# Performance work log

Measured on AMD Instinct MI355X. Metric: run time of the kernel, lower is better.

The kernel has to match this reference:

```python
import jax, jax.numpy as jnp
import numpy as np

BS, NE, NN, CIN, H, D = 8, 4800, 4981, 3, 128, 6
EPG = 19200
NEDGE = BS * EPG
N = BS * NE

PARAM_NAMES = [
    'enc_cw1','enc_cb1','enc_cw2','enc_cb2','enc_cw3','enc_clng','enc_clnb',
    'enc_ew1','enc_eb1','enc_ew2','enc_eb2','enc_ew3','enc_elng','enc_elnb',
    'p_ew1','p_eb1','p_ew2','p_eb2','p_ew3','p_elng','p_elnb',
    'p_nw1','p_nb1','p_nw2','p_nb2','p_nw3','p_nlng','p_nlnb',
    'dec_uw1','dec_ub1','dec_uw2','dec_ub2','dec_uw3','dec_ulng','dec_ulnb',
    'dec_cw1','dec_cb1','dec_cw2','dec_cb2','dec_cw3']


def setup_inputs():
    key = jax.random.key(0)
    ks = iter(jax.random.split(key, 64))
    def nrm(shape, s=0.1):
        return jax.random.normal(next(ks), shape, jnp.float32) * s
    inp = {}
    inp['x'] = jax.random.normal(next(ks), (BS * NN, CIN), jnp.float32)
    inp['elem_conn'] = jax.random.randint(next(ks), (NE, 4), 0, NN)
    inp['edge_index'] = jax.random.randint(next(ks), (2, NEDGE), 0, N)
    inp['enc_cw1'] = nrm((CIN, 4, 1)); inp['enc_cb1'] = nrm((CIN, 1), 0.01)
    inp['enc_cw2'] = nrm((CIN, 1, 1)); inp['enc_cb2'] = nrm((CIN, 1), 0.01)
    inp['enc_cw3'] = nrm((CIN, 1, 1))
    inp['enc_clng'] = jnp.ones((CIN, 1)); inp['enc_clnb'] = jnp.zeros((CIN, 1))
    inp['enc_ew1'] = nrm((CIN, H)); inp['enc_eb1'] = nrm((H,), 0.01)
    inp['enc_ew2'] = nrm((H, H)); inp['enc_eb2'] = nrm((H,), 0.01)
    inp['enc_ew3'] = nrm((H, H))
    inp['enc_elng'] = jnp.ones((H,)); inp['enc_elnb'] = jnp.zeros((H,))
    inp['p_ew1'] = nrm((D, 2 * H, H)); inp['p_eb1'] = nrm((D, H), 0.01)
    inp['p_ew2'] = nrm((D, H, H)); inp['p_eb2'] = nrm((D, H), 0.01)
    inp['p_ew3'] = nrm((D, H, H))
    inp['p_elng'] = jnp.ones((D, H)); inp['p_elnb'] = jnp.zeros((D, H))
    inp['p_nw1'] = nrm((D, 2 * H, H)); inp['p_nb1'] = nrm((D, H), 0.01)
    inp['p_nw2'] = nrm((D, H, H)); inp['p_nb2'] = nrm((D, H), 0.01)
    inp['p_nw3'] = nrm((D, H, H))
    inp['p_nlng'] = jnp.ones((D, H)); inp['p_nlnb'] = jnp.zeros((D, H))
    inp['dec_uw1'] = nrm((H, 1, 4)); inp['dec_ub1'] = nrm((H, 4), 0.01)
    inp['dec_uw2'] = nrm((H, 4, 4)); inp['dec_ub2'] = nrm((H, 4), 0.01)
    inp['dec_uw3'] = nrm((H, 4, 4))
    inp['dec_ulng'] = jnp.ones((H, 4)); inp['dec_ulnb'] = jnp.zeros((H, 4))
    inp['dec_cw1'] = nrm((H, CIN)); inp['dec_cb1'] = nrm((CIN,), 0.01)
    inp['dec_cw2'] = nrm((CIN, CIN)); inp['dec_cb2'] = nrm((CIN,), 0.01)
    inp['dec_cw3'] = nrm((CIN, CIN))
    return inp


def lrelu(x):
    return jnp.where(x >= 0, x, 0.2 * x)


def ln(x, g, b, axis=-1):
    m = jnp.mean(x, axis=axis, keepdims=True)
    v = jnp.var(x, axis=axis, keepdims=True)
    return (x - m) / jnp.sqrt(v + 1e-5) * g + b


def mlp(x, w1, b1, w2, b2, w3):
    h = lrelu(x @ w1 + b1)
    h = lrelu(h @ w2 + b2)
    return h @ w3


def _forward(fl, elem_conn, edge_index):
    x = fl[0]
    P = dict(zip(PARAM_NAMES, fl[1:]))
    # ---- Encoder: MeshCNN gather (4 mesh nodes per element) + per-channel MLP 4->1 ----
    xg = x.reshape(BS, NN, CIN)[:, elem_conn]                  # (BS, NE, 4, CIN)
    h = lrelu(jnp.einsum('beic,cio->beoc', xg, P['enc_cw1']) + P['enc_cb1'].T[None, None])
    h = lrelu(jnp.einsum('beic,cio->beoc', h, P['enc_cw2']) + P['enc_cb2'].T[None, None])
    h = jnp.einsum('beic,cio->beoc', h, P['enc_cw3'])
    h = ln(h, P['enc_clng'].T[None, None], P['enc_clnb'].T[None, None], axis=2)  # LayerNorm(1)
    h = h[:, :, 0, :].reshape(N, CIN)
    h = ln(mlp(h, P['enc_ew1'], P['enc_eb1'], P['enc_ew2'], P['enc_eb2'], P['enc_ew3']),
           P['enc_elng'], P['enc_elnb'])                       # (N, H)
    # ---- Processor: D GraphNet blocks, edge MLP + scatter-add + node MLP ----
    src, dest = edge_index[0], edge_index[1]
    stacked = (P['p_ew1'], P['p_eb1'], P['p_ew2'], P['p_eb2'], P['p_ew3'], P['p_elng'], P['p_elnb'],
               P['p_nw1'], P['p_nb1'], P['p_nw2'], P['p_nb2'], P['p_nw3'], P['p_nlng'], P['p_nlnb'])
    def step(hc, p):
        ew1, eb1, ew2, eb2, ew3, eg, ebv, nw1, nb1, nw2, nb2, nw3, ng, nbv = p
        msg = jnp.concatenate([hc[dest], hc[src]], axis=-1)    # (NEDGE, 2H)
        m = ln(mlp(msg, ew1, eb1, ew2, eb2, ew3), eg, ebv)
        aggr = jax.ops.segment_sum(m, dest, num_segments=N)
        hn = ln(mlp(jnp.concatenate([hc, aggr], axis=-1), nw1, nb1, nw2, nb2, nw3), ng, nbv)
        return hn, None
    h, _ = jax.lax.scan(step, h, stacked)
    # ---- Decoder: per-channel upsample 1->4 then index_add back to mesh nodes ----
    u = h.reshape(BS, NE, H)[:, :, None, :]                    # (BS, NE, 1, H)
    u = lrelu(jnp.einsum('beic,cio->beoc', u, P['dec_uw1']) + P['dec_ub1'].T[None, None])
    u = lrelu(jnp.einsum('beic,cio->beoc', u, P['dec_uw2']) + P['dec_ub2'].T[None, None])
    u = jnp.einsum('beic,cio->beoc', u, P['dec_uw3'])
    u = ln(u, P['dec_ulng'].T[None, None], P['dec_ulnb'].T[None, None], axis=2)  # (BS, NE, 4, H)
    out = jnp.zeros((BS, NN, H), u.dtype).at[:, elem_conn.reshape(-1)].add(u.reshape(BS, NE * 4, H))
    out = out.reshape(BS * NN, H)
    o = lrelu(out @ P['dec_cw1'] + P['dec_cb1'])
    o = lrelu(o @ P['dec_cw2'] + P['dec_cb2'])
    return o @ P['dec_cw3']


def reference(x, elem_conn, edge_index,
              enc_cw1, enc_cb1, enc_cw2, enc_cb2, enc_cw3, enc_clng, enc_clnb,
              enc_ew1, enc_eb1, enc_ew2, enc_eb2, enc_ew3, enc_elng, enc_elnb,
              p_ew1, p_eb1, p_ew2, p_eb2, p_ew3, p_elng, p_elnb,
              p_nw1, p_nb1, p_nw2, p_nb2, p_nw3, p_nlng, p_nlnb,
              dec_uw1, dec_ub1, dec_uw2, dec_ub2, dec_uw3, dec_ulng, dec_ulnb,
              dec_cw1, dec_cb1, dec_cw2, dec_cb2, dec_cw3):
    fl = (x, enc_cw1, enc_cb1, enc_cw2, enc_cb2, enc_cw3, enc_clng, enc_clnb,
          enc_ew1, enc_eb1, enc_ew2, enc_eb2, enc_ew3, enc_elng, enc_elnb,
          p_ew1, p_eb1, p_ew2, p_eb2, p_ew3, p_elng, p_elnb,
          p_nw1, p_nb1, p_nw2, p_nb2, p_nw3, p_nlng, p_nlnb,
          dec_uw1, dec_ub1, dec_uw2, dec_ub2, dec_uw3, dec_ulng, dec_ulnb,
          dec_cw1, dec_cb1, dec_cw2, dec_cb2, dec_cw3)
    return _forward(fl, elem_conn, edge_index)
```

## Files before the change

kernel.cpp:

```cpp
#include <hip/hip_runtime.h>
#include <hip/hip_fp16.h>
#include <math.h>

#define BS    8
#define NE    4800
#define NN    4981
#define CIN   3
#define HD    128
#define DBLK  6
#define NEDGE 153600
#define NTOT  38400
#define NMESH (BS*NN)
#define NNP   5120
#define EM    128

#define UW1T  0
#define UB1T  512
#define UW2T  1024
#define UB2T  3072
#define UW3T  3584
#define ULNGT 5632
#define ULNBT 6144
#define DWT_N 6656

typedef _Float16 f16;
typedef _Float16 f16x8 __attribute__((ext_vector_type(8)));
typedef float f32x4 __attribute__((ext_vector_type(4)));

__device__ __forceinline__ float lrelu(float x) { return x >= 0.0f ? x : 0.2f * x; }

__global__ __launch_bounds__(128)
void enc_msg0_kernel(const float* __restrict__ clnb,
                     const float* __restrict__ ew1, const float* __restrict__ eb1,
                     const float* __restrict__ ew2, const float* __restrict__ eb2,
                     const float* __restrict__ ew3,
                     const float* __restrict__ g, const float* __restrict__ b,
                     float* __restrict__ hv0,
                     const float* __restrict__ pew1, const float* __restrict__ peb1,
                     const float* __restrict__ pew2, const float* __restrict__ peb2,
                     const float* __restrict__ pew3,
                     const float* __restrict__ pg, const float* __restrict__ pb,
                     float* __restrict__ m0) {
    __shared__ float s1[HD], s2[HD], s3[HD], hv[HD];
    int j = threadIdx.x;
    float a = eb1[j];
    for (int c = 0; c < CIN; ++c) a += clnb[c] * ew1[c * HD + j];
    s1[j] = lrelu(a);
    __syncthreads();
    a = eb2[j];
    for (int k = 0; k < HD; ++k) a += s1[k] * ew2[k * HD + j];
    s2[j] = lrelu(a);
    __syncthreads();
    a = 0.0f;
    for (int k = 0; k < HD; ++k) a += s2[k] * ew3[k * HD + j];
    s3[j] = a;
    __syncthreads();
    float m = 0.0f;
    for (int k = 0; k < HD; ++k) m += s3[k];
    m *= (1.0f / HD);
    float v = 0.0f;
    for (int k = 0; k < HD; ++k) { float d = s3[k] - m; v += d * d; }
    v *= (1.0f / HD);
    float rs = 1.0f / sqrtf(v + 1e-5f);
    float h0 = (s3[j] - m) * rs * g[j] + b[j];
    hv0[j] = h0;
    hv[j] = h0;
    __syncthreads();
    a = peb1[j];
    for (int k = 0; k < HD; ++k) a += hv[k] * (pew1[k * HD + j] + pew1[(k + HD) * HD + j]);
    s1[j] = lrelu(a);
    __syncthreads();
    a = peb2[j];
    for (int k = 0; k < HD; ++k) a += s1[k] * pew2[k * HD + j];
    s2[j] = lrelu(a);
    __syncthreads();
    a = 0.0f;
    for (int k = 0; k < HD; ++k) a += s2[k] * pew3[k * HD + j];
    s3[j] = a;
    __syncthreads();
    m = 0.0f;
    for (int k = 0; k < HD; ++k) m += s3[k];
    m *= (1.0f / HD);
    v = 0.0f;
    for (int k = 0; k < HD; ++k) { float d = s3[k] - m; v += d * d; }
    v *= (1.0f / HD);
    rs = 1.0f / sqrtf(v + 1e-5f);
    m0[j] = (s3[j] - m) * rs * pg[j] + pb[j];
}

__global__ __launch_bounds__(256)
void conv_all_kernel(const float* __restrict__ ew1, const float* __restrict__ ew2,
                     const float* __restrict__ ew3,
                     const float* __restrict__ nw1, const float* __restrict__ nw2,
                     const float* __restrict__ nw3, f16* __restrict__ wbuf,
                     const float* __restrict__ eb1, f16* __restrict__ eb16) {
    int b = blockIdx.x;
    if (b == 48) {
        for (int i = threadIdx.x; i < DBLK * HD; i += 256)
            eb16[i] = (f16)eb1[i];
        return;
    }
    int d = b >> 3, m = b & 7;
    const float* src;
    switch (m) {
        case 0: src = ew1 + (size_t)d * 2 * HD * HD; break;
        case 1: src = ew1 + (size_t)d * 2 * HD * HD + HD * HD; break;
        case 2: src = ew2 + (size_t)d * HD * HD; break;
        case 3: src = ew3 + (size_t)d * HD * HD; break;
        case 4: src = nw1 + (size_t)d * 2 * HD * HD; break;
        case 5: src = nw1 + (size_t)d * 2 * HD * HD + HD * HD; break;
        case 6: src = nw2 + (size_t)d * HD * HD; break;
        default: src = nw3 + (size_t)d * HD * HD; break;
    }
    f16* out = wbuf + (size_t)b * HD * HD;
    for (int idx = threadIdx.x; idx < HD * HD; idx += 256) {
        int n = idx >> 7, k = idx & 127;
        out[idx] = (f16)src[k * HD + n];
    }
}

__global__ __launch_bounds__(256)
void conv_dec_weights(const float* __restrict__ uw1, const float* __restrict__ ub1,
                      const float* __restrict__ uw2, const float* __restrict__ ub2,
                      const float* __restrict__ uw3, const float* __restrict__ ulng,
                      const float* __restrict__ ulnb, float* __restrict__ dwt) {
    int tid = threadIdx.x;
    for (int idx = tid; idx < 512; idx += 256) {
        int o = idx >> 7, c = idx & 127;
        dwt[UW1T + idx] = uw1[c * 4 + o];
        dwt[UB1T + idx] = ub1[c * 4 + o];
        dwt[UB2T + idx] = ub2[c * 4 + o];
        dwt[ULNGT + idx] = ulng[c * 4 + o];
        dwt[ULNBT + idx] = ulnb[c * 4 + o];
    }
    for (int idx = tid; idx < 2048; idx += 256) {
        int io = idx >> 7, c = idx & 127;
        dwt[UW2T + idx] = uw2[c * 16 + io];
        dwt[UW3T + idx] = uw3[c * 16 + io];
    }
}

#define EHB (NEDGE / 256)
#define MHB (NE * 4 / 256)
#define ESB (NTOT / 256)
#define MSB (NNP / 256)

__global__ __launch_bounds__(256)
void prep_hist(const int* __restrict__ e_dst, const int* __restrict__ conn,
               int* __restrict__ deg, int* __restrict__ mdeg) {
    int b = blockIdx.x;
    if (b < EHB) {
        int e = b * 256 + threadIdx.x;
        atomicAdd(&deg[e_dst[e]], 1);
    } else {
        int idx = (b - EHB) * 256 + threadIdx.x;
        atomicAdd(&mdeg[conn[idx]], 1);
    }
}

__device__ __forceinline__ void scan1_body(const int* __restrict__ deg,
                                           int* __restrict__ rowptr,
                                           int* __restrict__ bsum, int bi) {
    __shared__ int s[256];
    int i = bi * 256 + threadIdx.x;
    int v = deg[i];
    s[threadIdx.x] = v;
    __syncthreads();
    for (int off = 1; off < 256; off <<= 1) {
        int t = (threadIdx.x >= off) ? s[threadIdx.x - off] : 0;
        __syncthreads();
        s[threadIdx.x] += t;
        __syncthreads();
    }
    rowptr[i] = s[threadIdx.x] - v;
    if (threadIdx.x == 255) bsum[bi] = s[255];
}

__global__ __launch_bounds__(256)
void prep_scan1(const int* __restrict__ deg, int* __restrict__ rowptr,
                int* __restrict__ bsum,
                const int* __restrict__ mdeg, int* __restrict__ mrow,
                int* __restrict__ mbsum) {
    int b = blockIdx.x;
    if (b < ESB) scan1_body(deg, rowptr, bsum, b);
    else         scan1_body(mdeg, mrow, mbsum, b - ESB);
}

__device__ __forceinline__ void scan2_body(int* __restrict__ bsum, int nb) {
    __shared__ int s[256];
    int v = (threadIdx.x < nb) ? bsum[threadIdx.x] : 0;
    s[threadIdx.x] = v;
    __syncthreads();
    for (int off = 1; off < 256; off <<= 1) {
        int t = (threadIdx.x >= off) ? s[threadIdx.x - off] : 0;
        __syncthreads();
        s[threadIdx.x] += t;
        __syncthreads();
    }
    if (threadIdx.x < nb) bsum[threadIdx.x] = s[threadIdx.x] - v;
}

__global__ __launch_bounds__(256)
void prep_scan2(int* __restrict__ bsum, int* __restrict__ mbsum) {
    if (blockIdx.x == 0) scan2_body(bsum, ESB);
    else                 scan2_body(mbsum, MSB);
}

__global__ __launch_bounds__(256)
void prep_scan3(int* __restrict__ rowptr, const int* __restrict__ bsum,
                int* __restrict__ mrow, const int* __restrict__ mbsum) {
    int b = blockIdx.x;
    if (b < ESB) {
        int i = b * 256 + threadIdx.x;
        rowptr[i] += bsum[b];
    } else {
        int i = (b - ESB) * 256 + threadIdx.x;
        mrow[i] += mbsum[b - ESB];
    }
}

__global__ __launch_bounds__(256)
void prep_scatter(const int* __restrict__ dest, const int* __restrict__ srcv,
                  const int* __restrict__ rowptr, int* __restrict__ cursor,
                  int* __restrict__ dsorted, int* __restrict__ ssorted,
                  const int* __restrict__ conn, const int* __restrict__ mrow,
                  int* __restrict__ mcur, int* __restrict__ mslot) {
    int b = blockIdx.x;
    if (b < EHB) {
        int e = b * 256 + threadIdx.x;
        int d = dest[e];
        int pos = rowptr[d] + atomicAdd(&cursor[d], 1);
        dsorted[pos] = d;
        ssorted[pos] = srcv[e];
    } else {
        int idx = (b - EHB) * 256 + threadIdx.x;
        int nd = conn[idx];
        int pos = mrow[nd] + atomicAdd(&mcur[nd], 1);
        mslot[pos] = idx;
    }
}

template <int NT>
__device__ __forceinline__ void stage_w(const f16* __restrict__ Wg, f16 (*Bt)[HD + 8],
                                        int tid) {
    #pragma unroll
    for (int t = 0; t < 2048 / NT; ++t) {
        int idx = tid + t * NT;
        int r = idx >> 4, c = (idx & 15) * 8;
        *(uint4*)(&Bt[r][c]) = *(const uint4*)(Wg + (size_t)r * HD + c);
    }
}

__device__ __forceinline__ void mfma_pass(const f16 (*A)[HD + 8], const f16 (*Bt)[HD + 8],
                                          int rt_base, int ct_base, int ln, int quad,
                                          f32x4 acc[2][4]) {
    #pragma unroll
    for (int ks = 0; ks < 4; ++ks) {
        int kb = ks * 32 + quad * 8;
        f16x8 a0 = *(const f16x8*)(&A[rt_base + ln][kb]);
        f16x8 a1 = *(const f16x8*)(&A[rt_base + 16 + ln][kb]);
        #pragma unroll
        for (int c = 0; c < 4; ++c) {
            f16x8 b = *(const f16x8*)(&Bt[ct_base + c * 16 + ln][kb]);
            acc[0][c] = __builtin_amdgcn_mfma_f32_16x16x32_f16(a0, b, acc[0][c], 0, 0, 0);
            acc[1][c] = __builtin_amdgcn_mfma_f32_16x16x32_f16(a1, b, acc[1][c], 0, 0, 0);
        }
    }
}

__global__ __launch_bounds__(512, 4)
void gn_edge(const f16* __restrict__ P1, const f16* __restrict__ P2,
             const int* __restrict__ dsorted, const int* __restrict__ ssorted,
             const f16* __restrict__ W2, const f16* __restrict__ W3,
             const f16* __restrict__ b1h, const float* __restrict__ b2,
             const float* __restrict__ g, const float* __restrict__ bln,
             f16* __restrict__ msg) {
    __shared__ __align__(16) f16 As[EM][HD + 8];
    __shared__ __align__(16) f16 Bt[HD][HD + 8];
    __shared__ float red[EM][2][2];

    const int tid = threadIdx.x;
    const int base = blockIdx.x * EM;
    const int wave = tid >> 6, lane = tid & 63;
    const int ln = lane & 15, quad = lane >> 4;
    const int rt_base = (wave >> 1) * 32;
    const int ct_base = (wave & 1) * 64;
    const int half = wave & 1;
    const int r0 = tid >> 4;
    const int cg = (tid & 15) * 8;

    const f16 k02s = (f16)0.2f;
    const f16x8 k02 = {k02s, k02s, k02s, k02s, k02s, k02s, k02s, k02s};

    int dI[4], sI[4];
    #pragma unroll
    for (int it = 0; it < 4; ++it) {
        dI[it] = dsorted[base + r0 + it * 32];
        sI[it] = ssorted[base + r0 + it * 32];
    }
    stage_w<512>(W2, Bt, tid);
    const f16x8 bb = *(const f16x8*)(b1h + cg);
    #pragma unroll
    for (int it = 0; it < 4; ++it) {
        f16x8 p1 = *(const f16x8*)(P1 + (size_t)dI[it] * HD + cg);
        f16x8 p2 = *(const f16x8*)(P2 + (size_t)sI[it] * HD + cg);
        f16x8 s = p1 + p2 + bb;
        *(f16x8*)(&As[r0 + it * 32][cg]) = __builtin_elementwise_max(s, s * k02);
    }
    __syncthreads();

    f32x4 acc[2][4];

    #pragma unroll
    for (int c = 0; c < 4; ++c) {
        float bj = b2[ct_base + c * 16 + ln];
        f32x4 bv = {bj, bj, bj, bj};
        acc[0][c] = bv; acc[1][c] = bv;
    }
    mfma_pass(As, Bt, rt_base, ct_base, ln, quad, acc);
    __syncthreads();
    stage_w<512>(W3, Bt, tid);
    #pragma unroll
    for (int i = 0; i < 2; ++i)
        #pragma unroll
        for (int c = 0; c < 4; ++c)
            #pragma unroll
            for (int r = 0; r < 4; ++r)
                As[rt_base + i * 16 + quad * 4 + r][ct_base + c * 16 + ln] =
                    (f16)lrelu(acc[i][c][r]);
    __syncthreads();

    #pragma unroll
    for (int c = 0; c < 4; ++c) { f32x4 z = {0,0,0,0}; acc[0][c] = z; acc[1][c] = z; }
    mfma_pass(As, Bt, rt_base, ct_base, ln, quad, acc);

    #pragma unroll
    for (int i = 0; i < 2; ++i)
        #pragma unroll
        for (int r = 0; r < 4; ++r) {
            float s = acc[i][0][r] + acc[i][1][r] + acc[i][2][r] + acc[i][3][r];
            float q = acc[i][0][r] * acc[i][0][r] + acc[i][1][r] * acc[i][1][r] +
                      acc[i][2][r] * acc[i][2][r] + acc[i][3][r] * acc[i][3][r];
            s += __shfl_xor(s, 1); q += __shfl_xor(q, 1);
            s += __shfl_xor(s, 2); q += __shfl_xor(q, 2);
            s += __shfl_xor(s, 4); q += __shfl_xor(q, 4);
            s += __shfl_xor(s, 8); q += __shfl_xor(q, 8);
            if (ln == 0) {
                int row = rt_base + i * 16 + quad * 4 + r;
                red[row][half][0] = s;
                red[row][half][1] = q;
            }
        }
    __syncthreads();

    float gv[4], bv[4];
    #pragma unroll
    for (int c = 0; c < 4; ++c) {
        int col = ct_base + c * 16 + ln;
        gv[c] = g[col]; bv[c] = bln[col];
    }
    #pragma unroll
    for (int i = 0; i < 2; ++i)
        #pragma unroll
        for (int r = 0; r < 4; ++r) {
            int row = rt_base + i * 16 + quad * 4 + r;
            float s = red[row][0][0] + red[row][1][0];
            float q = red[row][0][1] + red[row][1][1];
            float m = s * (1.0f / HD);
            float var = q * (1.0f / HD) - m * m;
            float rs = 1.0f / sqrtf(var + 1e-5f);
            #pragma unroll
            for (int c = 0; c < 4; ++c) {
                int col = ct_base + c * 16 + ln;
                float v = (acc[i][c][r] - m) * rs * gv[c] + bv[c];
                msg[(size_t)(base + row) * HD + col] = (f16)v;
            }
        }
}

template <int AGGR, bool PROD>
__global__ __launch_bounds__(256, 3)
void gn_node(f16* __restrict__ h16, const f16* __restrict__ msg,
             const int* __restrict__ rowptr, const int* __restrict__ deg,
             const float* __restrict__ m0, const float* __restrict__ hv0,
             const f16* __restrict__ W1a, const f16* __restrict__ W1b,
             const f16* __restrict__ W2, const f16* __restrict__ W3,
             const float* __restrict__ b1, const float* __restrict__ b2,
             const float* __restrict__ g, const float* __restrict__ bln,
             const f16* __restrict__ nW1a, const f16* __restrict__ nW1b,
             f16* __restrict__ P1, f16* __restrict__ P2) {
    __shared__ __align__(16) f16 As[64][HD + 8];
    __shared__ __align__(16) f16 Bt[HD][HD + 8];
    __shared__ float red[64][2][2];

    const int tid = threadIdx.x;
    const int base = blockIdx.x * 64;
    const int wave = tid >> 6, lane = tid & 63;
    const int ln = lane & 15, quad = lane >> 4;
    const int rt_base = (wave >> 1) * 32;
    const int ct_base = (wave & 1) * 64;
    const int half = wave & 1;

    f16x8 hreg[4];
    #pragma unroll
    for (int t = 0; t < 4; ++t) {
        int r = (tid >> 4) + t * 16;
        int c = (tid & 15) * 8;
        if (AGGR == 0) {
            f16x8 hz;
            #pragma unroll
            for (int u = 0; u < 8; ++u) hz[u] = (f16)hv0[c + u];
            hreg[t] = hz;
            float sc = (float)deg[base + r];
            f16x8 o;
            #pragma unroll
            for (int u = 0; u < 8; ++u) o[u] = (f16)(sc * m0[c + u]);
            *(f16x8*)(&As[r][c]) = o;
        } else {
            hreg[t] = *(const f16x8*)(h16 + (size_t)(base + r) * HD + c);
            int rp = rowptr[base + r], dg = deg[base + r];
            float a[8] = {0, 0, 0, 0, 0, 0, 0, 0};
            int j = 0;
            for (; j + 4 <= dg; j += 4) {
                f16x8 v0 = *(const f16x8*)(msg + (size_t)(rp + j) * HD + c);
                f16x8 v1 = *(const f16x8*)(msg + (size_t)(rp + j + 1) * HD + c);
                f16x8 v2 = *(const f16x8*)(msg + (size_t)(rp + j + 2) * HD + c);
                f16x8 v3 = *(const f16x8*)(msg + (size_t)(rp + j + 3) * HD + c);
                #pragma unroll
                for (int u = 0; u < 8; ++u)
                    a[u] += ((float)v0[u] + (float)v1[u]) + ((float)v2[u] + (float)v3[u]);
            }
            for (; j < dg; ++j) {
                f16x8 mv = *(const f16x8*)(msg + (size_t)(rp + j) * HD + c);
                #pragma unroll
                for (int u = 0; u < 8; ++u) a[u] += (float)mv[u];
            }
            f16x8 o;
            #pragma unroll
            for (int u = 0; u < 8; ++u) o[u] = (f16)a[u];
            *(f16x8*)(&As[r][c]) = o;
        }
    }
    stage_w<256>(W1b, Bt, tid);
    __syncthreads();

    f32x4 acc[2][4];
    #pragma unroll
    for (int c = 0; c < 4; ++c) {
        float bj = b1[ct_base + c * 16 + ln];
        f32x4 bb = {bj, bj, bj, bj};
        acc[0][c] = bb; acc[1][c] = bb;
    }
    mfma_pass(As, Bt, rt_base, ct_base, ln, quad, acc);
    __syncthreads();

    #pragma unroll
    for (int t = 0; t < 4; ++t) {
        int r = (tid >> 4) + t * 16;
        int c = (tid & 15) * 8;
        *(f16x8*)(&As[r][c]) = hreg[t];
    }
    stage_w<256>(W1a, Bt, tid);
    __syncthreads();
    mfma_pass(As, Bt, rt_base, ct_base, ln, quad, acc);
    __syncthreads();

    stage_w<256>(W2, Bt, tid);
    #pragma unroll
    for (int i = 0; i < 2; ++i)
        #pragma unroll
        for (int c = 0; c < 4; ++c)
            #pragma unroll
            for (int r = 0; r < 4; ++r)
                As[rt_base + i * 16 + quad * 4 + r][ct_base + c * 16 + ln] =
                    (f16)lrelu(acc[i][c][r]);
    __syncthreads();

    #pragma unroll
    for (int c = 0; c < 4; ++c) {
        float bj = b2[ct_base + c * 16 + ln];
        f32x4 bb = {bj, bj, bj, bj};
        acc[0][c] = bb; acc[1][c] = bb;
    }
    mfma_pass(As, Bt, rt_base, ct_base, ln, quad, acc);
    __syncthreads();
    stage_w<256>(W3, Bt, tid);
    #pragma unroll
    for (int i = 0; i < 2; ++i)
        #pragma unroll
        for (int c = 0; c < 4; ++c)
            #pragma unroll
            for (int r = 0; r < 4; ++r)
                As[rt_base + i * 16 + quad * 4 + r][ct_base + c * 16 + ln] =
                    (f16)lrelu(acc[i][c][r]);
    __syncthreads();

    #pragma unroll
    for (int c = 0; c < 4; ++c) { f32x4 z = {0,0,0,0}; acc[0][c] = z; acc[1][c] = z; }
    mfma_pass(As, Bt, rt_base, ct_base, ln, quad, acc);

    #pragma unroll
    for (int i = 0; i < 2; ++i)
        #pragma unroll
        for (int r = 0; r < 4; ++r) {
            float s = acc[i][0][r] + acc[i][1][r] + acc[i][2][r] + acc[i][3][r];
            float q = acc[i][0][r] * acc[i][0][r] + acc[i][1][r] * acc[i][1][r] +
                      acc[i][2][r] * acc[i][2][r] + acc[i][3][r] * acc[i][3][r];
            s += __shfl_xor(s, 1); q += __shfl_xor(q, 1);
            s += __shfl_xor(s, 2); q += __shfl_xor(q, 2);
            s += __shfl_xor(s, 4); q += __shfl_xor(q, 4);
            s += __shfl_xor(s, 8); q += __shfl_xor(q, 8);
            if (ln == 0) {
                int row = rt_base + i * 16 + quad * 4 + r;
                red[row][half][0] = s;
                red[row][half][1] = q;
            }
        }
    __syncthreads();

    float gv[4], bv[4];
    #pragma unroll
    for (int c = 0; c < 4; ++c) {
        int col = ct_base + c * 16 + ln;
        gv[c] = g[col]; bv[c] = bln[col];
    }
    #pragma unroll
    for (int i = 0; i < 2; ++i)
        #pragma unroll
        for (int r = 0; r < 4; ++r) {
            int row = rt_base + i * 16 + quad * 4 + r;
            float s = red[row][0][0] + red[row][1][0];
            float q = red[row][0][1] + red[row][1][1];
            float m = s * (1.0f / HD);
            float var = q * (1.0f / HD) - m * m;
            float rs = 1.0f / sqrtf(var + 1e-5f);
            #pragma unroll
            for (int c = 0; c < 4; ++c) {
                int col = ct_base + c * 16 + ln;
                float v = (acc[i][c][r] - m) * rs * gv[c] + bv[c];
                f16 hv = (f16)v;
                h16[(size_t)(base + row) * HD + col] = hv;
                if (PROD) As[row][col] = hv;
            }
        }

    if (PROD) {
        __syncthreads();
        stage_w<256>(nW1a, Bt, tid);
        __syncthreads();
        #pragma unroll
        for (int c = 0; c < 4; ++c) { f32x4 z = {0,0,0,0}; acc[0][c] = z; acc[1][c] = z; }
        mfma_pass(As, Bt, rt_base, ct_base, ln, quad, acc);
        #pragma unroll
        for (int i = 0; i < 2; ++i)
            #pragma unroll
            for (int c = 0; c < 4; ++c)
                #pragma unroll
                for (int r = 0; r < 4; ++r)
                    P1[(size_t)(base + rt_base + i * 16 + quad * 4 + r) * HD +
                       ct_base + c * 16 + ln] = (f16)acc[i][c][r];
        __syncthreads();
        stage_w<256>(nW1b, Bt, tid);
        __syncthreads();
        #pragma unroll
        for (int c = 0; c < 4; ++c) { f32x4 z = {0,0,0,0}; acc[0][c] = z; acc[1][c] = z; }
        mfma_pass(As, Bt, rt_base, ct_base, ln, quad, acc);
        #pragma unroll
        for (int i = 0; i < 2; ++i)
            #pragma unroll
            for (int c = 0; c < 4; ++c)
                #pragma unroll
                for (int r = 0; r < 4; ++r)
                    P2[(size_t)(base + rt_base + i * 16 + quad * 4 + r) * HD +
                       ct_base + c * 16 + ln] = (f16)acc[i][c][r];
    }
}

__global__ __launch_bounds__(256)
void dec_store_kernel(const f16* __restrict__ h, const float* __restrict__ dwt,
                      f16* __restrict__ uval) {
    __shared__ f16 ub[2][4][HD];
    int tid = threadIdx.x;
    int idx = blockIdx.x * 256 + tid;
    int c = idx & 127;
    int nl = tid >> 7;
    float s = (float)h[idx];
    float u1[4], u2[4], u3[4];
    #pragma unroll
    for (int o = 0; o < 4; ++o)
        u1[o] = lrelu(s * dwt[UW1T + o * 128 + c] + dwt[UB1T + o * 128 + c]);
    #pragma unroll
    for (int o = 0; o < 4; ++o) {
        float a = dwt[UB2T + o * 128 + c];
        #pragma unroll
        for (int i = 0; i < 4; ++i) a += u1[i] * dwt[UW2T + (i * 4 + o) * 128 + c];
        u2[o] = lrelu(a);
    }
    #pragma unroll
    for (int o = 0; o < 4; ++o) {
        float a = 0.f;
        #pragma unroll
        for (int i = 0; i < 4; ++i) a += u2[i] * dwt[UW3T + (i * 4 + o) * 128 + c];
        u3[o] = a;
    }
    float m = 0.25f * (u3[0] + u3[1] + u3[2] + u3[3]);
    float var = 0.f;
    #pragma unroll
    for (int o = 0; o < 4; ++o) { float d = u3[o] - m; var += d * d; }
    var *= 0.25f;
    float rs = 1.0f / sqrtf(var + 1e-5f);
    #pragma unroll
    for (int o = 0; o < 4; ++o) {
        float val = (u3[o] - m) * rs * dwt[ULNGT + o * 128 + c] + dwt[ULNBT + o * 128 + c];
        ub[nl][o][c] = (f16)val;
    }
    __syncthreads();
    int nl2 = tid >> 7, rem = tid & 127;
    uint2 v = ((const uint2*)&ub[nl2][0][0])[rem];
    ((uint2*)(uval + (size_t)(blockIdx.x * 2 + nl2) * 4 * HD))[rem] = v;
}

__global__ __launch_bounds__(256)
void dec_gather_out(const f16* __restrict__ uval,
                    const int* __restrict__ mrow, const int* __restrict__ mdeg,
                    const int* __restrict__ mslot,
                    const float* __restrict__ cw1, const float* __restrict__ cb1,
                    const float* __restrict__ cw2, const float* __restrict__ cb2,
                    const float* __restrict__ cw3,
                    float* __restrict__ o, int nrows) {
    int r = blockIdx.x * 4 + (threadIdx.x >> 6);
    if (r >= nrows) return;
    int lane = threadIdx.x & 63;
    int b = r / NN, n = r - b * NN;
    int rp = mrow[n], dg = mdeg[n];
    size_t boff = (size_t)b * NE * 4;
    float a0 = 0.f, a1 = 0.f;
    for (int j = 0; j < dg; ++j) {
        int slot = mslot[rp + j];
        const f16* up = uval + (boff + slot) * HD + lane * 2;
        a0 += (float)up[0];
        a1 += (float)up[1];
    }
    int c0 = lane * 2, c1 = lane * 2 + 1;
    float s[3];
    #pragma unroll
    for (int k = 0; k < 3; ++k)
        s[k] = a0 * cw1[c0 * 3 + k] + a1 * cw1[c1 * 3 + k];
    #pragma unroll
    for (int off = 32; off >= 1; off >>= 1) {
        s[0] += __shfl_down(s[0], off);
        s[1] += __shfl_down(s[1], off);
        s[2] += __shfl_down(s[2], off);
    }
    if (lane == 0) {
        float t1[3], t2[3];
        #pragma unroll
        for (int k = 0; k < 3; ++k) t1[k] = lrelu(s[k] + cb1[k]);
        #pragma unroll
        for (int k = 0; k < 3; ++k) {
            float a = cb2[k];
            #pragma unroll
            for (int q = 0; q < 3; ++q) a += t1[q] * cw2[q * 3 + k];
            t2[k] = lrelu(a);
        }
        #pragma unroll
        for (int k = 0; k < 3; ++k) {
            float a = 0.f;
            #pragma unroll
            for (int q = 0; q < 3; ++q) a += t2[q] * cw3[q * 3 + k];
            o[(size_t)r * 3 + k] = a;
        }
    }
}

extern "C" void kernel_launch(void* const* d_in, const int* in_sizes, int n_in,
                              void* d_out, int out_size, void* d_ws, size_t ws_size,
                              hipStream_t stream) {
    const int* elem_conn = (const int*)d_in[1];
    const int* edge_index = (const int*)d_in[2];
    const int* e_src = edge_index;
    const int* e_dst = edge_index + NEDGE;
    const float* enc_clnb = (const float*)d_in[9];
    const float* enc_ew1 = (const float*)d_in[10];
    const float* enc_eb1 = (const float*)d_in[11];
    const float* enc_ew2 = (const float*)d_in[12];
    const float* enc_eb2 = (const float*)d_in[13];
    const float* enc_ew3 = (const float*)d_in[14];
    const float* enc_elng = (const float*)d_in[15];
    const float* enc_elnb = (const float*)d_in[16];
    const float* p_ew1 = (const float*)d_in[17];
    const float* p_eb1 = (const float*)d_in[18];
    const float* p_ew2 = (const float*)d_in[19];
    const float* p_eb2 = (const float*)d_in[20];
    const float* p_ew3 = (const float*)d_in[21];
    const float* p_elng = (const float*)d_in[22];
    const float* p_elnb = (const float*)d_in[23];
    const float* p_nw1 = (const float*)d_in[24];
    const float* p_nb1 = (const float*)d_in[25];
    const float* p_nw2 = (const float*)d_in[26];
    const float* p_nb2 = (const float*)d_in[27];
    const float* p_nw3 = (const float*)d_in[28];
    const float* p_nlng = (const float*)d_in[29];
    const float* p_nlnb = (const float*)d_in[30];
    const float* dec_uw1 = (const float*)d_in[31];
    const float* dec_ub1 = (const float*)d_in[32];
    const float* dec_uw2 = (const float*)d_in[33];
    const float* dec_ub2 = (const float*)d_in[34];
    const float* dec_uw3 = (const float*)d_in[35];
    const float* dec_ulng = (const float*)d_in[36];
    const float* dec_ulnb = (const float*)d_in[37];
    const float* dec_cw1 = (const float*)d_in[38];
    const float* dec_cb1 = (const float*)d_in[39];
    const float* dec_cw2 = (const float*)d_in[40];
    const float* dec_cb2 = (const float*)d_in[41];
    const float* dec_cw3 = (const float*)d_in[42];

    char* ws = (char*)d_ws;
    f16*   h16     = (f16*)(ws);
    f16*   wbuf    = (f16*)(ws + 9830400);
    float* hv0     = (float*)(ws + 11403264);
    float* m0      = (float*)(ws + 11403776);
    f16*   P1      = (f16*)(ws + 11404288);
    f16*   P2      = (f16*)(ws + 21234688);
    f16*   msg     = (f16*)(ws + 31065088);
    f16*   uval    = (f16*)(ws + 31065088);
    int*   deg     = (int*)(ws + 70386688);
    int*   rowptr  = (int*)(ws + 70540288);
    int*   cursor  = (int*)(ws + 70693888);
    int*   bsum    = (int*)(ws + 70847488);
    int*   dsorted = (int*)(ws + 70848512);
    int*   ssorted = (int*)(ws + 71462912);
    f16*   eb16    = (f16*)(ws + 72077312);
    int*   mdeg    = (int*)(ws + 72078848);
    int*   mrow    = (int*)(ws + 72099328);
    int*   mcur    = (int*)(ws + 72119808);
    int*   mbsum   = (int*)(ws + 72140288);
    int*   mslot   = (int*)(ws + 72141312);
    float* dwt     = (float*)P1;

    hipMemsetAsync(deg, 0, 72218112 - 70386688, stream);

    enc_msg0_kernel<<<1, 128, 0, stream>>>(
        enc_clnb, enc_ew1, enc_eb1, enc_ew2, enc_eb2, enc_ew3, enc_elng, enc_elnb, hv0,
        p_ew1, p_eb1, p_ew2, p_eb2, p_ew3, p_elng, p_elnb, m0);
    conv_all_kernel<<<49, 256, 0, stream>>>(p_ew1, p_ew2, p_ew3,
                                            p_nw1, p_nw2, p_nw3, wbuf, p_eb1, eb16);

    prep_hist<<<EHB + MHB, 256, 0, stream>>>(e_dst, elem_conn, deg, mdeg);
    prep_scan1<<<ESB + MSB, 256, 0, stream>>>(deg, rowptr, bsum, mdeg, mrow, mbsum);
    prep_scan2<<<2, 256, 0, stream>>>(bsum, mbsum);
    prep_scan3<<<ESB + MSB, 256, 0, stream>>>(rowptr, bsum, mrow, mbsum);
    prep_scatter<<<EHB + MHB, 256, 0, stream>>>(e_dst, e_src, rowptr, cursor,
                                                dsorted, ssorted,
                                                elem_conn, mrow, mcur, mslot);

    {
        const f16* wd = wbuf;
        const f16* wn = wbuf + (size_t)8 * HD * HD;
        gn_node<0, true><<<NTOT / 64, 256, 0, stream>>>(
            h16, nullptr, nullptr, deg, m0, hv0,
            wd + 4 * HD * HD, wd + 5 * HD * HD, wd + 6 * HD * HD, wd + 7 * HD * HD,
            p_nb1, p_nb2, p_nlng, p_nlnb,
            wn + 0 * HD * HD, wn + 1 * HD * HD, P1, P2);
    }

    for (int d = 1; d < DBLK; ++d) {
        const f16* wd = wbuf + (size_t)d * 8 * HD * HD;
        gn_edge<<<NEDGE / EM, 512, 0, stream>>>(
            P1, P2, dsorted, ssorted,
            wd + 2 * HD * HD, wd + 3 * HD * HD,
            eb16 + (size_t)d * HD, p_eb2 + (size_t)d * HD,
            p_elng + (size_t)d * HD, p_elnb + (size_t)d * HD, msg);
        if (d < DBLK - 1) {
            const f16* wn = wbuf + (size_t)(d + 1) * 8 * HD * HD;
            gn_node<1, true><<<NTOT / 64, 256, 0, stream>>>(
                h16, msg, rowptr, deg, nullptr, nullptr,
                wd + 4 * HD * HD, wd + 5 * HD * HD, wd + 6 * HD * HD, wd + 7 * HD * HD,
                p_nb1 + (size_t)d * HD, p_nb2 + (size_t)d * HD,
                p_nlng + (size_t)d * HD, p_nlnb + (size_t)d * HD,
                wn + 0 * HD * HD, wn + 1 * HD * HD, P1, P2);
        } else {
            gn_node<1, false><<<NTOT / 64, 256, 0, stream>>>(
                h16, msg, rowptr, deg, nullptr, nullptr,
                wd + 4 * HD * HD, wd + 5 * HD * HD, wd + 6 * HD * HD, wd + 7 * HD * HD,
                p_nb1 + (size_t)d * HD, p_nb2 + (size_t)d * HD,
                p_nlng + (size_t)d * HD, p_nlnb + (size_t)d * HD,
                wbuf, wbuf, P1, P2);
        }
    }

    conv_dec_weights<<<1, 256, 0, stream>>>(dec_uw1, dec_ub1, dec_uw2, dec_ub2,
                                            dec_uw3, dec_ulng, dec_ulnb, dwt);
    dec_store_kernel<<<NTOT * HD / 256, 256, 0, stream>>>(h16, dwt, uval);
    dec_gather_out<<<(NMESH + 3) / 4, 256, 0, stream>>>(
        uval, mrow, mdeg, mslot, dec_cw1, dec_cb1, dec_cw2, dec_cb2, dec_cw3,
        (float*)d_out, NMESH);
}
```

Measured before the change: 600.8 us.

## Fuse decoder element MLP into final node kernel and merge weight-conversion launch

The final gn_node pass now runs the per-channel decoder MLP and its LayerNorm directly on the freshly normalized node features and writes uval itself. This removes the separate dec_store kernel along with its h16 round trip. The decoder weight transpose moves into an extra block of conv_all_kernel, saving a launch, and dwt and uval get their own workspace regions. dec_gather_out also unrolls its gather loop by four to expose more memory-level parallelism. In exchange the fused epilogue raises register pressure in gn_node and writes uval through strided scalar stores.

```diff
diff --git a/kernel.cpp b/kernel.cpp
--- a/kernel.cpp
+++ b/kernel.cpp
@@ -93,11 +93,32 @@
                      const float* __restrict__ ew3,
                      const float* __restrict__ nw1, const float* __restrict__ nw2,
                      const float* __restrict__ nw3, f16* __restrict__ wbuf,
-                     const float* __restrict__ eb1, f16* __restrict__ eb16) {
+                     const float* __restrict__ eb1, f16* __restrict__ eb16,
+                     const float* __restrict__ uw1, const float* __restrict__ ub1,
+                     const float* __restrict__ uw2, const float* __restrict__ ub2,
+                     const float* __restrict__ uw3, const float* __restrict__ ulng,
+                     const float* __restrict__ ulnb, float* __restrict__ dwt) {
     int b = blockIdx.x;
+    int tid = threadIdx.x;
     if (b == 48) {
-        for (int i = threadIdx.x; i < DBLK * HD; i += 256)
+        for (int i = tid; i < DBLK * HD; i += 256)
             eb16[i] = (f16)eb1[i];
+        return;
+    }
+    if (b == 49) {
+        for (int idx = tid; idx < 512; idx += 256) {
+            int o = idx >> 7, c = idx & 127;
+            dwt[UW1T + idx] = uw1[c * 4 + o];
+            dwt[UB1T + idx] = ub1[c * 4 + o];
+            dwt[UB2T + idx] = ub2[c * 4 + o];
+            dwt[ULNGT + idx] = ulng[c * 4 + o];
+            dwt[ULNBT + idx] = ulnb[c * 4 + o];
+        }
+        for (int idx = tid; idx < 2048; idx += 256) {
+            int io = idx >> 7, c = idx & 127;
+            dwt[UW2T + idx] = uw2[c * 16 + io];
+            dwt[UW3T + idx] = uw3[c * 16 + io];
+        }
         return;
     }
     int d = b >> 3, m = b & 7;
@@ -113,30 +134,9 @@
         default: src = nw3 + (size_t)d * HD * HD; break;
     }
     f16* out = wbuf + (size_t)b * HD * HD;
-    for (int idx = threadIdx.x; idx < HD * HD; idx += 256) {
+    for (int idx = tid; idx < HD * HD; idx += 256) {
         int n = idx >> 7, k = idx & 127;
         out[idx] = (f16)src[k * HD + n];
-    }
-}
-
-__global__ __launch_bounds__(256)
-void conv_dec_weights(const float* __restrict__ uw1, const float* __restrict__ ub1,
-                      const float* __restrict__ uw2, const float* __restrict__ ub2,
-                      const float* __restrict__ uw3, const float* __restrict__ ulng,
-                      const float* __restrict__ ulnb, float* __restrict__ dwt) {
-    int tid = threadIdx.x;
-    for (int idx = tid; idx < 512; idx += 256) {
-        int o = idx >> 7, c = idx & 127;
-        dwt[UW1T + idx] = uw1[c * 4 + o];
-        dwt[UB1T + idx] = ub1[c * 4 + o];
-        dwt[UB2T + idx] = ub2[c * 4 + o];
-        dwt[ULNGT + idx] = ulng[c * 4 + o];
-        dwt[ULNBT + idx] = ulnb[c * 4 + o];
-    }
-    for (int idx = tid; idx < 2048; idx += 256) {
-        int io = idx >> 7, c = idx & 127;
-        dwt[UW2T + idx] = uw2[c * 16 + io];
-        dwt[UW3T + idx] = uw3[c * 16 + io];
     }
 }
 
@@ -378,7 +378,7 @@
         }
 }
 
-template <int AGGR, bool PROD>
+template <int AGGR, bool PROD, bool DECF>
 __global__ __launch_bounds__(256, 3)
 void gn_node(f16* __restrict__ h16, const f16* __restrict__ msg,
              const int* __restrict__ rowptr, const int* __restrict__ deg,
@@ -388,7 +388,8 @@
              const float* __restrict__ b1, const float* __restrict__ b2,
              const float* __restrict__ g, const float* __restrict__ bln,
              const f16* __restrict__ nW1a, const f16* __restrict__ nW1b,
-             f16* __restrict__ P1, f16* __restrict__ P2) {
+             f16* __restrict__ P1, f16* __restrict__ P2,
+             const float* __restrict__ dwt, f16* __restrict__ uval) {
     __shared__ __align__(16) f16 As[64][HD + 8];
     __shared__ __align__(16) f16 Bt[HD][HD + 8];
     __shared__ float red[64][2][2];
@@ -524,25 +525,98 @@
         int col = ct_base + c * 16 + ln;
         gv[c] = g[col]; bv[c] = bln[col];
     }
-    #pragma unroll
-    for (int i = 0; i < 2; ++i)
-        #pragma unroll
-        for (int r = 0; r < 4; ++r) {
-            int row = rt_base + i * 16 + quad * 4 + r;
-            float s = red[row][0][0] + red[row][1][0];
-            float q = red[row][0][1] + red[row][1][1];
-            float m = s * (1.0f / HD);
-            float var = q * (1.0f / HD) - m * m;
-            float rs = 1.0f / sqrtf(var + 1e-5f);
-            #pragma unroll
-            for (int c = 0; c < 4; ++c) {
-                int col = ct_base + c * 16 + ln;
-                float v = (acc[i][c][r] - m) * rs * gv[c] + bv[c];
-                f16 hv = (f16)v;
-                h16[(size_t)(base + row) * HD + col] = hv;
-                if (PROD) As[row][col] = hv;
+
+    if (!DECF) {
+        #pragma unroll
+        for (int i = 0; i < 2; ++i)
+            #pragma unroll
+            for (int r = 0; r < 4; ++r) {
+                int row = rt_base + i * 16 + quad * 4 + r;
+                float s = red[row][0][0] + red[row][1][0];
+                float q = red[row][0][1] + red[row][1][1];
+                float m = s * (1.0f / HD);
+                float var = q * (1.0f / HD) - m * m;
+                float rs = 1.0f / sqrtf(var + 1e-5f);
+                #pragma unroll
+                for (int c = 0; c < 4; ++c) {
+                    int col = ct_base + c * 16 + ln;
+                    float v = (acc[i][c][r] - m) * rs * gv[c] + bv[c];
+                    f16 hv = (f16)v;
+                    h16[(size_t)(base + row) * HD + col] = hv;
+                    if (PROD) As[row][col] = hv;
+                }
             }
-        }
+    } else {
+        float mm[2][4], rr[2][4];
+        #pragma unroll
+        for (int i = 0; i < 2; ++i)
+            #pragma unroll
+            for (int r = 0; r < 4; ++r) {
+                int row = rt_base + i * 16 + quad * 4 + r;
+                float s = red[row][0][0] + red[row][1][0];
+                float q = red[row][0][1] + red[row][1][1];
+                float m = s * (1.0f / HD);
+                float var = q * (1.0f / HD) - m * m;
+                mm[i][r] = m;
+                rr[i][r] = 1.0f / sqrtf(var + 1e-5f);
+            }
+        #pragma unroll
+        for (int c = 0; c < 4; ++c) {
+            int col = ct_base + c * 16 + ln;
+            float w1v[4], wb1[4], wb2[4], lg4[4], lb4[4];
+            #pragma unroll
+            for (int o = 0; o < 4; ++o) {
+                w1v[o] = dwt[UW1T + o * 128 + col];
+                wb1[o] = dwt[UB1T + o * 128 + col];
+                wb2[o] = dwt[UB2T + o * 128 + col];
+                lg4[o] = dwt[ULNGT + o * 128 + col];
+                lb4[o] = dwt[ULNBT + o * 128 + col];
+            }
+            float w2v[16], w3v[16];
+            #pragma unroll
+            for (int io = 0; io < 16; ++io) {
+                w2v[io] = dwt[UW2T + io * 128 + col];
+                w3v[io] = dwt[UW3T + io * 128 + col];
+            }
+            #pragma unroll
+            for (int i = 0; i < 2; ++i)
+                #pragma unroll
+                for (int r = 0; r < 4; ++r) {
+                    int row = rt_base + i * 16 + quad * 4 + r;
+                    float v = (acc[i][c][r] - mm[i][r]) * rr[i][r] * gv[c] + bv[c];
+                    float s = (float)(f16)v;
+                    float u1[4], u2[4], u3[4];
+                    #pragma unroll
+                    for (int o = 0; o < 4; ++o)
+                        u1[o] = lrelu(s * w1v[o] + wb1[o]);
+                    #pragma unroll
+                    for (int o = 0; o < 4; ++o) {
+                        float a = wb2[o];
+                        #pragma unroll
+                        for (int i2 = 0; i2 < 4; ++i2) a += u1[i2] * w2v[i2 * 4 + o];
+                        u2[o] = lrelu(a);
+                    }
+                    #pragma unroll
+                    for (int o = 0; o < 4; ++o) {
+                        float a = 0.f;
+                        #pragma unroll
+                        for (int i2 = 0; i2 < 4; ++i2) a += u2[i2] * w3v[i2 * 4 + o];
+                        u3[o] = a;
+                    }
+                    float m4 = 0.25f * (u3[0] + u3[1] + u3[2] + u3[3]);
+                    float var4 = 0.f;
+                    #pragma unroll
+                    for (int o = 0; o < 4; ++o) { float d = u3[o] - m4; var4 += d * d; }
+                    var4 *= 0.25f;
+                    float rs4 = 1.0f / sqrtf(var4 + 1e-5f);
+                    size_t ub = (size_t)(base + row) * 4 * HD + col;
+                    #pragma unroll
+                    for (int o = 0; o < 4; ++o)
+                        uval[ub + (size_t)o * HD] =
+                            (f16)((u3[o] - m4) * rs4 * lg4[o] + lb4[o]);
+                }
+        }
+    }
 
     if (PROD) {
         __syncthreads();
@@ -574,50 +648,6 @@
                     P2[(size_t)(base + rt_base + i * 16 + quad * 4 + r) * HD +
                        ct_base + c * 16 + ln] = (f16)acc[i][c][r];
     }
-}
-
-__global__ __launch_bounds__(256)
-void dec_store_kernel(const f16* __restrict__ h, const float* __restrict__ dwt,
-                      f16* __restrict__ uval) {
-    __shared__ f16 ub[2][4][HD];
-    int tid = threadIdx.x;
-    int idx = blockIdx.x * 256 + tid;
-    int c = idx & 127;
-    int nl = tid >> 7;
-    float s = (float)h[idx];
-    float u1[4], u2[4], u3[4];
-    #pragma unroll
-    for (int o = 0; o < 4; ++o)
-        u1[o] = lrelu(s * dwt[UW1T + o * 128 + c] + dwt[UB1T + o * 128 + c]);
-    #pragma unroll
-    for (int o = 0; o < 4; ++o) {
-        float a = dwt[UB2T + o * 128 + c];
-        #pragma unroll
-        for (int i = 0; i < 4; ++i) a += u1[i] * dwt[UW2T + (i * 4 + o) * 128 + c];
-        u2[o] = lrelu(a);
-    }
-    #pragma unroll
-    for (int o = 0; o < 4; ++o) {
-        float a = 0.f;
-        #pragma unroll
-        for (int i = 0; i < 4; ++i) a += u2[i] * dwt[UW3T + (i * 4 + o) * 128 + c];
-        u3[o] = a;
-    }
-    float m = 0.25f * (u3[0] + u3[1] + u3[2] + u3[3]);
-    float var = 0.f;
-    #pragma unroll
-    for (int o = 0; o < 4; ++o) { float d = u3[o] - m; var += d * d; }
-    var *= 0.25f;
-    float rs = 1.0f / sqrtf(var + 1e-5f);
-    #pragma unroll
-    for (int o = 0; o < 4; ++o) {
-        float val = (u3[o] - m) * rs * dwt[ULNGT + o * 128 + c] + dwt[ULNBT + o * 128 + c];
-        ub[nl][o][c] = (f16)val;
-    }
-    __syncthreads();
-    int nl2 = tid >> 7, rem = tid & 127;
-    uint2 v = ((const uint2*)&ub[nl2][0][0])[rem];
-    ((uint2*)(uval + (size_t)(blockIdx.x * 2 + nl2) * 4 * HD))[rem] = v;
 }
 
 __global__ __launch_bounds__(256)
@@ -635,7 +665,22 @@
     int rp = mrow[n], dg = mdeg[n];
     size_t boff = (size_t)b * NE * 4;
     float a0 = 0.f, a1 = 0.f;
-    for (int j = 0; j < dg; ++j) {
+    int j = 0;
+    for (; j + 4 <= dg; j += 4) {
+        int s0 = mslot[rp + j], s1 = mslot[rp + j + 1];
+        int s2 = mslot[rp + j + 2], s3 = mslot[rp + j + 3];
+        const f16* u0 = uval + (boff + s0) * HD + lane * 2;
+        const f16* u1 = uval + (boff + s1) * HD + lane * 2;
+        const f16* u2 = uval + (boff + s2) * HD + lane * 2;
+        const f16* u3 = uval + (boff + s3) * HD + lane * 2;
+        float b00 = (float)u0[0], b01 = (float)u0[1];
+        float b10 = (float)u1[0], b11 = (float)u1[1];
+        float b20 = (float)u2[0], b21 = (float)u2[1];
+        float b30 = (float)u3[0], b31 = (float)u3[1];
+        a0 += (b00 + b10) + (b20 + b30);
+        a1 += (b01 + b11) + (b21 + b31);
+    }
+    for (; j < dg; ++j) {
         int slot = mslot[rp + j];
         const f16* up = uval + (boff + slot) * HD + lane * 2;
         a0 += (float)up[0];
@@ -723,7 +768,6 @@
     f16*   P1      = (f16*)(ws + 11404288);
     f16*   P2      = (f16*)(ws + 21234688);
     f16*   msg     = (f16*)(ws + 31065088);
-    f16*   uval    = (f16*)(ws + 31065088);
     int*   deg     = (int*)(ws + 70386688);
     int*   rowptr  = (int*)(ws + 70540288);
     int*   cursor  = (int*)(ws + 70693888);
@@ -736,15 +780,18 @@
     int*   mcur    = (int*)(ws + 72119808);
     int*   mbsum   = (int*)(ws + 72140288);
     int*   mslot   = (int*)(ws + 72141312);
-    float* dwt     = (float*)P1;
+    float* dwt     = (float*)(ws + 72218112);
+    f16*   uval    = (f16*)(ws + 72244736);
 
     hipMemsetAsync(deg, 0, 72218112 - 70386688, stream);
 
     enc_msg0_kernel<<<1, 128, 0, stream>>>(
         enc_clnb, enc_ew1, enc_eb1, enc_ew2, enc_eb2, enc_ew3, enc_elng, enc_elnb, hv0,
         p_ew1, p_eb1, p_ew2, p_eb2, p_ew3, p_elng, p_elnb, m0);
-    conv_all_kernel<<<49, 256, 0, stream>>>(p_ew1, p_ew2, p_ew3,
-                                            p_nw1, p_nw2, p_nw3, wbuf, p_eb1, eb16);
+    conv_all_kernel<<<50, 256, 0, stream>>>(p_ew1, p_ew2, p_ew3,
+                                            p_nw1, p_nw2, p_nw3, wbuf, p_eb1, eb16,
+                                            dec_uw1, dec_ub1, dec_uw2, dec_ub2,
+                                            dec_uw3, dec_ulng, dec_ulnb, dwt);
 
     prep_hist<<<EHB + MHB, 256, 0, stream>>>(e_dst, elem_conn, deg, mdeg);
     prep_scan1<<<ESB + MSB, 256, 0, stream>>>(deg, rowptr, bsum, mdeg, mrow, mbsum);
@@ -757,11 +804,11 @@
     {
         const f16* wd = wbuf;
         const f16* wn = wbuf + (size_t)8 * HD * HD;
-        gn_node<0, true><<<NTOT / 64, 256, 0, stream>>>(
+        gn_node<0, true, false><<<NTOT / 64, 256, 0, stream>>>(
             h16, nullptr, nullptr, deg, m0, hv0,
             wd + 4 * HD * HD, wd + 5 * HD * HD, wd + 6 * HD * HD, wd + 7 * HD * HD,
             p_nb1, p_nb2, p_nlng, p_nlnb,
-            wn + 0 * HD * HD, wn + 1 * HD * HD, P1, P2);
+            wn + 0 * HD * HD, wn + 1 * HD * HD, P1, P2, nullptr, nullptr);
     }
 
     for (int d = 1; d < DBLK; ++d) {
@@ -773,25 +820,22 @@
             p_elng + (size_t)d * HD, p_elnb + (size_t)d * HD, msg);
         if (d < DBLK - 1) {
             const f16* wn = wbuf + (size_t)(d + 1) * 8 * HD * HD;
-            gn_node<1, true><<<NTOT / 64, 256, 0, stream>>>(
+            gn_node<1, true, false><<<NTOT / 64, 256, 0, stream>>>(
                 h16, msg, rowptr, deg, nullptr, nullptr,
                 wd + 4 * HD * HD, wd + 5 * HD * HD, wd + 6 * HD * HD, wd + 7 * HD * HD,
                 p_nb1 + (size_t)d * HD, p_nb2 + (size_t)d * HD,
                 p_nlng + (size_t)d * HD, p_nlnb + (size_t)d * HD,
-                wn + 0 * HD * HD, wn + 1 * HD * HD, P1, P2);
+                wn + 0 * HD * HD, wn + 1 * HD * HD, P1, P2, nullptr, nullptr);
         } else {
-            gn_node<1, false><<<NTOT / 64, 256, 0, stream>>>(
+            gn_node<1, false, true><<<NTOT / 64, 256, 0, stream>>>(
                 h16, msg, rowptr, deg, nullptr, nullptr,
                 wd + 4 * HD * HD, wd + 5 * HD * HD, wd + 6 * HD * HD, wd + 7 * HD * HD,
                 p_nb1 + (size_t)d * HD, p_nb2 + (size_t)d * HD,
                 p_nlng + (size_t)d * HD, p_nlnb + (size_t)d * HD,
-                wbuf, wbuf, P1, P2);
-        }
-    }
-
-    conv_dec_weights<<<1, 256, 0, stream>>>(dec_uw1, dec_ub1, dec_uw2, dec_ub2,
-                                            dec_uw3, dec_ulng, dec_ulnb, dwt);
-    dec_store_kernel<<<NTOT * HD / 256, 256, 0, stream>>>(h16, dwt, uval);
+                wbuf, wbuf, P1, P2, dwt, uval);
+        }
+    }
+
     dec_gather_out<<<(NMESH + 3) / 4, 256, 0, stream>>>(
         uval, mrow, mdeg, mslot, dec_cw1, dec_cb1, dec_cw2, dec_cb2, dec_cw3,
         (float*)d_out, NMESH);
```

Measured after the change: 578.4 us. -3.7%, faster.
